# Kernel optimization log

Hardware: AMD Instinct MI355X
Metric: run time of the kernel (lower is better)

## Reference

```python
import jax, jax.numpy as jnp
import numpy as np

NUM_HEADS = 16
KEY_DIM = 64
EPS = 1e-6


def setup_inputs() -> dict:
    key = jax.random.key(0)
    k0, k1, k2, k3, k4 = jax.random.split(key, 5)
    B, S, E = 4, 4096, NUM_HEADS * KEY_DIM
    scale = 1.0 / np.sqrt(KEY_DIM)
    return {
        "query": jax.random.normal(k0, (B, S, E), dtype=jnp.float32),
        "Wq": jax.random.normal(k1, (NUM_HEADS, KEY_DIM, KEY_DIM), dtype=jnp.float32) * scale,
        "Wk": jax.random.normal(k2, (NUM_HEADS, KEY_DIM, KEY_DIM), dtype=jnp.float32) * scale,
        "Wv": jax.random.normal(k3, (NUM_HEADS, KEY_DIM, KEY_DIM), dtype=jnp.float32) * scale,
        "Wo": jax.random.normal(k4, (E, E), dtype=jnp.float32) * (1.0 / np.sqrt(E)),
    }


def reference(query, Wq, Wk, Wv, Wo):
    # Self-attention: key = value = query (per call() defaults).
    B, S, E = query.shape
    H, D = NUM_HEADS, KEY_DIM
    # split_heads: (B, S, E) -> (B, H, S, D)
    x = jnp.transpose(query.reshape(B, S, H, D), (0, 2, 1, 3))
    # Per-head linear projections (all heads batched in one einsum each).
    q = jnp.einsum("bhsd,hde->bhse", x, Wq)
    k = jnp.einsum("bhsd,hde->bhse", x, Wk)
    v = jnp.einsum("bhsd,hde->bhse", x, Wv)
    # Kernel feature map phi(x) = elu(x) + 1 (strictly positive).
    phi_q = jax.nn.elu(q) + 1.0
    phi_k = jax.nn.elu(k) + 1.0
    # Linear (non-causal) attention: O(S*D^2) instead of O(S^2*D).
    kv = jnp.einsum("bhsd,bhse->bhde", phi_k, v)        # (B,H,D,D)
    k_sum = jnp.sum(phi_k, axis=2)                       # (B,H,D)
    z = jnp.einsum("bhsd,bhd->bhs", phi_q, k_sum)        # (B,H,S)
    ctx = jnp.einsum("bhsd,bhde->bhse", phi_q, kv) / (z[..., None] + EPS)
    # combine_heads: (B,H,S,D) -> (B,S,E), then output projection (no bias).
    combined = jnp.transpose(ctx, (0, 2, 1, 3)).reshape(B, S, H * D)
    return combined @ Wo
```

## Files before the change

kernel.cpp:

```cpp
#include <hip/hip_runtime.h>
#include <stdint.h>

#define S_LEN 4096
#define NHEADS 16
#define DHEAD 64
#define EMB 1024
#define NBATCH 4
#define NBH (NBATCH * NHEADS)

typedef unsigned short u16t;
typedef __attribute__((ext_vector_type(8))) short short8;
typedef __attribute__((ext_vector_type(4))) float f32x4;

__device__ __forceinline__ u16t f2bf(float f) {
  unsigned int x = __float_as_uint(f);
  x += 0x7fffu + ((x >> 16) & 1u);
  return (u16t)(x >> 16);
}
__device__ __forceinline__ unsigned int pack2(float a, float b) {
  return (unsigned int)f2bf(a) | ((unsigned int)f2bf(b) << 16);
}
__device__ __forceinline__ float bf2f(u16t u) { return __uint_as_float(((unsigned int)u) << 16); }
__device__ __forceinline__ float phifn(float v) { return v > 0.f ? v + 1.f : __expf(v); }

__device__ __forceinline__ void stage_w8k(const u16t* __restrict__ wg,
                                          u16t* __restrict__ lds, int t) {
#pragma unroll
  for (int c = 0; c < 2; ++c) {
    const u16t* src = wg + (size_t)(c * 256 + t) * 8;
    char* dst = (char*)lds + c * 4096 + ((t >> 6) << 10);
    __builtin_amdgcn_global_load_lds((const __attribute__((address_space(1))) unsigned int*)src,
                                     (__attribute__((address_space(3))) unsigned int*)dst,
                                     16, 0, 0);
  }
}

__global__ __launch_bounds__(256) void la_wprep(const float* __restrict__ Wq,
                                                const float* __restrict__ Wk,
                                                const float* __restrict__ Wv,
                                                const float* __restrict__ Wo,
                                                u16t* __restrict__ WqT,
                                                u16t* __restrict__ WkT,
                                                u16t* __restrict__ WvT,
                                                u16t* __restrict__ WoT) {
  __shared__ float tmp[64][65];
  int blk = blockIdx.x;
  int t = threadIdx.x;
  if (blk < 48) {
    int mat = blk >> 4, h = blk & 15;
    const float* src = (mat == 0 ? Wq : (mat == 1 ? Wk : Wv)) + (size_t)h * 4096;
    u16t* dst = (mat == 0 ? WqT : (mat == 1 ? WkT : WvT)) + (size_t)h * 4096;
#pragma unroll
    for (int p = 0; p < 16; ++p) {
      int i = p * 256 + t;
      tmp[i >> 6][i & 63] = src[i];
    }
    __syncthreads();
#pragma unroll
    for (int p = 0; p < 16; ++p) {
      int i = p * 256 + t;
      int e = i >> 6, r = i & 63, o = r >> 3, j = r & 7;
      dst[i] = f2bf(tmp[((o ^ (e & 7)) << 3) + j][e]);
    }
  } else {
    int bb = blk - 48;
    int n0 = (bb & 15) * 64, k0 = (bb >> 4) * 64;
    int tx = t & 63, ty = t >> 6;
    for (int r = ty; r < 64; r += 4) tmp[r][tx] = Wo[(size_t)(k0 + r) * EMB + n0 + tx];
    __syncthreads();
    for (int r = ty; r < 64; r += 4)
      WoT[(size_t)(n0 + r) * EMB + k0 + tx] = f2bf(tmp[tx][r]);
  }
}

__global__ __launch_bounds__(256) void la_kvq5(const float* __restrict__ q,
                                               const u16t* __restrict__ WqT,
                                               const u16t* __restrict__ WkT,
                                               const u16t* __restrict__ WvT,
                                               u16t* __restrict__ phiq,
                                               float* __restrict__ kvpart,
                                               float* __restrict__ kspart) {
  __shared__ u16t xs[64 * 72];
  __shared__ u16t wq[4096];
  __shared__ u16t wk[4096];
  __shared__ u16t wv[4096];
  __shared__ u16t pkT[64 * 72];
  __shared__ u16t vT[64 * 72];
  __shared__ float ksp4[4][64];
  int blk = blockIdx.x;
  int bh = blk >> 3, tile = blk & 7;
  int b = bh >> 4, h = bh & 15;
  int s0 = tile << 9;
  int t = threadIdx.x;
  int wave = t >> 6, lane = t & 63, l16 = lane & 15, g = lane >> 4;

  stage_w8k(WqT + (size_t)h * 4096, wq, t);
  stage_w8k(WkT + (size_t)h * 4096, wk, t);
  stage_w8k(WvT + (size_t)h * 4096, wv, t);

  const float* xg = q + ((size_t)b * S_LEN + s0) * EMB + h * 64;
  int pr_r = t >> 4, pr_c4 = (t & 15) * 4;

  float4 pre[4];
#pragma unroll
  for (int i = 0; i < 4; ++i)
    pre[i] = *(const float4*)(xg + (size_t)(i * 16 + pr_r) * EMB + pr_c4);

  f32x4 kacc[4];
#pragma unroll
  for (int n = 0; n < 4; ++n) kacc[n] = 0.f;
  float ks_acc = 0.f;
  int ks_e = t & 63, ks_q = t >> 6;

  for (int c = 0; c < 8; ++c) {
    if (c) __syncthreads();
#pragma unroll
    for (int i = 0; i < 4; ++i) {
      uint2 p;
      p.x = pack2(pre[i].x, pre[i].y);
      p.y = pack2(pre[i].z, pre[i].w);
      *(uint2*)(&xs[(i * 16 + pr_r) * 72 + pr_c4]) = p;
    }
    if (c < 7) {
#pragma unroll
      for (int i = 0; i < 4; ++i)
        pre[i] = *(const float4*)(xg + (size_t)((c + 1) * 64 + i * 16 + pr_r) * EMB + pr_c4);
    }
    __syncthreads();

    f32x4 aQ[4], aK[4], aV[4];
#pragma unroll
    for (int n = 0; n < 4; ++n) { aQ[n] = 0.f; aK[n] = 0.f; aV[n] = 0.f; }
    short8 af[2];
#pragma unroll
    for (int kk = 0; kk < 2; ++kk)
      af[kk] = *(const short8*)(&xs[(wave * 16 + l16) * 72 + kk * 32 + g * 8]);
#pragma unroll
    for (int n = 0; n < 4; ++n) {
      int e = n * 16 + l16;
#pragma unroll
      for (int kk = 0; kk < 2; ++kk) {
        int op = (kk * 4 + g) ^ (l16 & 7);
        short8 bQ = *(const short8*)(&wq[e * 64 + op * 8]);
        short8 bK = *(const short8*)(&wk[e * 64 + op * 8]);
        short8 bV = *(const short8*)(&wv[e * 64 + op * 8]);
        aQ[n] = __builtin_amdgcn_mfma_f32_16x16x32_bf16(af[kk], bQ, aQ[n], 0, 0, 0);
        aK[n] = __builtin_amdgcn_mfma_f32_16x16x32_bf16(af[kk], bK, aK[n], 0, 0, 0);
        aV[n] = __builtin_amdgcn_mfma_f32_16x16x32_bf16(af[kk], bV, aV[n], 0, 0, 0);
      }
    }
    __syncthreads();

#pragma unroll
    for (int n = 0; n < 4; ++n) {
      int e = n * 16 + l16;
      int sb = wave * 16 + g * 4;
      uint2 pk2, vv2;
      pk2.x = pack2(phifn(aK[n][0]), phifn(aK[n][1]));
      pk2.y = pack2(phifn(aK[n][2]), phifn(aK[n][3]));
      vv2.x = pack2(aV[n][0], aV[n][1]);
      vv2.y = pack2(aV[n][2], aV[n][3]);
      *(uint2*)(&pkT[e * 72 + sb]) = pk2;
      *(uint2*)(&vT[e * 72 + sb]) = vv2;
#pragma unroll
      for (int j = 0; j < 4; ++j) xs[(sb + j) * 72 + e] = f2bf(phifn(aQ[n][j]));
    }
    __syncthreads();

#pragma unroll
    for (int i = 0; i < 2; ++i) {
      int slot = i * 256 + t;
      int r = slot >> 3, cc = (slot & 7) * 8;
      *(uint4*)(phiq + ((size_t)bh * S_LEN + s0 + c * 64 + r) * 64 + cc) =
          *(const uint4*)(&xs[r * 72 + cc]);
    }
#pragma unroll
    for (int ks = 0; ks < 2; ++ks) {
      short8 pa = *(const short8*)(&pkT[(wave * 16 + l16) * 72 + ks * 32 + g * 8]);
#pragma unroll
      for (int n = 0; n < 4; ++n) {
        short8 vb = *(const short8*)(&vT[(n * 16 + l16) * 72 + ks * 32 + g * 8]);
        kacc[n] = __builtin_amdgcn_mfma_f32_16x16x32_bf16(pa, vb, kacc[n], 0, 0, 0);
      }
    }
#pragma unroll
    for (int i = 0; i < 4; ++i) {
      uint2 u = *(const uint2*)(&pkT[ks_e * 72 + ks_q * 16 + i * 4]);
      ks_acc += bf2f((u16t)(u.x & 0xffff)) + bf2f((u16t)(u.x >> 16)) +
                bf2f((u16t)(u.y & 0xffff)) + bf2f((u16t)(u.y >> 16));
    }
  }

  float* kp = kvpart + (size_t)blk * 4096;
#pragma unroll
  for (int n = 0; n < 4; ++n)
#pragma unroll
    for (int j = 0; j < 4; ++j)
      kp[(wave * 16 + g * 4 + j) * 64 + n * 16 + l16] = kacc[n][j];

  ksp4[ks_q][ks_e] = ks_acc;
  __syncthreads();
  if (t < 64)
    kspart[(size_t)blk * 64 + t] = ksp4[0][t] + ksp4[1][t] + ksp4[2][t] + ksp4[3][t];
}

__global__ __launch_bounds__(256) void la_red3(const float* __restrict__ kvpart,
                                               const float* __restrict__ kspart,
                                               const u16t* __restrict__ WoT,
                                               float* __restrict__ ksum_g,
                                               u16t* __restrict__ W2T) {
  __shared__ float kvs[64][65];
  __shared__ u16t aT[256 * 72];
  int bh = blockIdx.x;
  int b = bh >> 4, h = bh & 15;
  int t = threadIdx.x, wave = t >> 6, lane = t & 63, l16 = lane & 15, g = lane >> 4;

  float acc[16];
#pragma unroll
  for (int i = 0; i < 16; ++i) acc[i] = 0.f;
  for (int p = 0; p < 8; ++p) {
    const float* base = kvpart + ((size_t)bh * 8 + p) * 4096;
#pragma unroll
    for (int i = 0; i < 16; ++i) acc[i] += base[i * 256 + t];
  }
#pragma unroll
  for (int i = 0; i < 16; ++i) {
    int idx = i * 256 + t;
    kvs[idx >> 6][idx & 63] = acc[i];
  }
  if (t < 64) {
    float a = 0.f;
    for (int p = 0; p < 8; ++p) a += kspart[((size_t)bh * 8 + p) * 64 + t];
    ksum_g[(size_t)bh * 64 + t] = a;
  }
  __syncthreads();

  short8 kvbf[4][2];
#pragma unroll
  for (int n = 0; n < 4; ++n)
#pragma unroll
    for (int kk = 0; kk < 2; ++kk) {
      u16t* pp = (u16t*)&kvbf[n][kk];
#pragma unroll
      for (int i = 0; i < 8; ++i) pp[i] = f2bf(kvs[n * 16 + l16][kk * 32 + g * 8 + i]);
    }

  for (int ec = 0; ec < 4; ++ec) {
    if (ec) __syncthreads();
#pragma unroll
    for (int p = 0; p < 8; ++p) {
      int slot = p * 256 + t;
      int r = slot >> 3, cc = (slot & 7) * 8;
      *(uint4*)(&aT[r * 72 + cc]) =
          *(const uint4*)(WoT + (size_t)(ec * 256 + r) * 1024 + h * 64 + cc);
    }
    __syncthreads();
    f32x4 c2[4][4];
#pragma unroll
    for (int mi = 0; mi < 4; ++mi)
#pragma unroll
      for (int n = 0; n < 4; ++n) c2[mi][n] = 0.f;
#pragma unroll
    for (int kk = 0; kk < 2; ++kk)
#pragma unroll
      for (int mi = 0; mi < 4; ++mi) {
        short8 afr = *(const short8*)(&aT[(wave * 64 + mi * 16 + l16) * 72 + kk * 32 + g * 8]);
#pragma unroll
        for (int n = 0; n < 4; ++n)
          c2[mi][n] = __builtin_amdgcn_mfma_f32_16x16x32_bf16(afr, kvbf[n][kk], c2[mi][n], 0, 0, 0);
      }
    __syncthreads();
#pragma unroll
    for (int mi = 0; mi < 4; ++mi)
#pragma unroll
      for (int n = 0; n < 4; ++n)
#pragma unroll
        for (int j = 0; j < 4; ++j)
          aT[(wave * 64 + mi * 16 + g * 4 + j) * 72 + n * 16 + l16] = f2bf(c2[mi][n][j]);
    __syncthreads();
#pragma unroll
    for (int p = 0; p < 8; ++p) {
      int slot = p * 256 + t;
      int r = slot >> 3, cc = (slot & 7) * 8;
      *(uint4*)(W2T + ((size_t)b << 20) + (size_t)(ec * 256 + r) * 1024 + h * 64 + cc) =
          *(const uint4*)(&aT[r * 72 + cc]);
    }
  }
}

__global__ __launch_bounds__(256) void la_scale(const u16t* __restrict__ phiq,
                                                const float* __restrict__ ksum_g,
                                                u16t* __restrict__ phiq2) {
  __shared__ float ks[64];
  int blk = blockIdx.x;
  int bh = blk >> 4, sl = blk & 15;
  int b = bh >> 4, h = bh & 15;
  int s0 = sl * 256;
  int t = threadIdx.x;
  if (t < 64) ks[t] = ksum_g[(size_t)bh * 64 + t];
  __syncthreads();
  int c16 = t & 15, rg = t >> 4;
#pragma unroll 2
  for (int it = 0; it < 16; ++it) {
    int s = s0 + it * 16 + rg;
    uint2 u = *(const uint2*)(phiq + ((size_t)bh * S_LEN + s) * 64 + c16 * 4);
    float f0 = bf2f((u16t)(u.x & 0xffff)), f1 = bf2f((u16t)(u.x >> 16));
    float f2 = bf2f((u16t)(u.y & 0xffff)), f3 = bf2f((u16t)(u.y >> 16));
    float zp = f0 * ks[c16 * 4] + f1 * ks[c16 * 4 + 1] + f2 * ks[c16 * 4 + 2] + f3 * ks[c16 * 4 + 3];
    zp += __shfl_xor(zp, 1);
    zp += __shfl_xor(zp, 2);
    zp += __shfl_xor(zp, 4);
    zp += __shfl_xor(zp, 8);
    float inv = 1.f / (zp + 1e-6f);
    uint2 o;
    o.x = pack2(f0 * inv, f1 * inv);
    o.y = pack2(f2 * inv, f3 * inv);
    *(uint2*)(phiq2 + ((size_t)(b * S_LEN + s)) * EMB + h * 64 + c16 * 4) = o;
  }
}

__device__ __forceinline__ void stage_half(const u16t* __restrict__ gbase,
                                           u16t* __restrict__ lbuf,
                                           int half, int t) {
#pragma unroll
  for (int it = 0; it < 2; ++it) {
    int slot = it * 512 + t;
    int row = half * 128 + (slot >> 3);
    int oct = slot & 7;
    const u16t* src = gbase + (size_t)row * EMB + (((oct ^ (row & 7)) << 3));
    char* dst = (char*)lbuf + ((half * 128 + it * 64 + ((t >> 6) << 3)) << 7);
    __builtin_amdgcn_global_load_lds((const __attribute__((address_space(1))) unsigned int*)src,
                                     (__attribute__((address_space(3))) unsigned int*)dst,
                                     16, 0, 0);
  }
}

#define GFENCE asm volatile("" ::: "memory")

#define LOAD_A(QM)                                                              \
  _Pragma("unroll") for (int mi = 0; mi < 4; ++mi) _Pragma("unroll")            \
      for (int kk = 0; kk < 2; ++kk) {                                          \
    int rr = (QM) * 128 + wr2 * 64 + mi * 16 + l16;                             \
    afr[mi][kk] = *(const short8*)((const char*)Acur + rr * 128 +               \
                                   ((((kk << 2) | g) ^ (rr & 7)) << 4));        \
  }
#define LOAD_B(QN, DST)                                                         \
  _Pragma("unroll") for (int ni = 0; ni < 2; ++ni) _Pragma("unroll")            \
      for (int kk = 0; kk < 2; ++kk) {                                          \
    int rr = (QN) * 128 + wc2 * 32 + ni * 16 + l16;                             \
    DST[ni][kk] = *(const short8*)((const char*)Bcur + rr * 128 +               \
                                   ((((kk << 2) | g) ^ (rr & 7)) << 4));        \
  }
#define MFMA_Q(QM, QN, BF)                                                      \
  __builtin_amdgcn_s_setprio(1);                                                \
  _Pragma("unroll") for (int mi = 0; mi < 4; ++mi) _Pragma("unroll")            \
      for (int ni = 0; ni < 2; ++ni) {                                          \
    acc[QM][QN][mi][ni] = __builtin_amdgcn_mfma_f32_16x16x32_bf16(              \
        afr[mi][0], BF[ni][0], acc[QM][QN][mi][ni], 0, 0, 0);                   \
    acc[QM][QN][mi][ni] = __builtin_amdgcn_mfma_f32_16x16x32_bf16(              \
        afr[mi][1], BF[ni][1], acc[QM][QN][mi][ni], 0, 0, 0);                   \
  }                                                                             \
  __builtin_amdgcn_s_setprio(0);

#define BAR()                      \
  __builtin_amdgcn_s_barrier();    \
  GFENCE

__global__ __launch_bounds__(512, 2) void la_gemm9(const u16t* __restrict__ A,
                                                   const u16t* __restrict__ W2T,
                                                   float* __restrict__ C) {
  __shared__ u16t SMEM[65536];
  u16t* Al0 = SMEM;
  u16t* Al1 = SMEM + 16384;
  u16t* Bl0 = SMEM + 32768;
  u16t* Bl1 = SMEM + 49152;
  int t = threadIdx.x;
  int bid = blockIdx.x;
  int swz = ((bid & 7) << 5) + (bid >> 3);
  int mt = swz >> 2, nt = swz & 3;
  const int M0 = mt * 256, N0 = nt * 256;
  const int b = mt >> 4;
  int wave = t >> 6, lane = t & 63;
  int l16 = lane & 15, g = lane >> 4;
  int wr2 = wave >> 2, wc2 = wave & 3;

  f32x4 acc[2][2][4][2];
#pragma unroll
  for (int qm = 0; qm < 2; ++qm)
#pragma unroll
    for (int qn = 0; qn < 2; ++qn)
#pragma unroll
      for (int mi = 0; mi < 4; ++mi)
#pragma unroll
        for (int ni = 0; ni < 2; ++ni) acc[qm][qn][mi][ni] = 0.f;

  const u16t* Asrc = A + (size_t)M0 * EMB;
  const u16t* Bsrc = W2T + ((size_t)b << 20) + (size_t)N0 * EMB;

  stage_half(Asrc, Al0, 0, t);
  stage_half(Bsrc, Bl0, 0, t);
  stage_half(Bsrc, Bl0, 1, t);
  stage_half(Asrc, Al0, 1, t);
  asm volatile("s_waitcnt vmcnt(4)" ::: "memory");
  BAR();

  short8 afr[4][2], bf0[2][2], bf1[2][2];

  for (int kt = 0; kt < 15; ++kt) {
    const u16t* Acur = (kt & 1) ? Al1 : Al0;
    const u16t* Bcur = (kt & 1) ? Bl1 : Bl0;
    u16t* Anxt = (kt & 1) ? Al0 : Al1;
    u16t* Bnxt = (kt & 1) ? Bl0 : Bl1;
    const u16t* An = Asrc + (kt + 1) * 64;
    const u16t* Bn = Bsrc + (kt + 1) * 64;
    LOAD_A(0);
    LOAD_B(0, bf0);
    stage_half(An, Anxt, 0, t);
    stage_half(Bn, Bnxt, 0, t);
    asm volatile("s_waitcnt vmcnt(6)" ::: "memory");
    BAR();
    MFMA_Q(0, 0, bf0);
    GFENCE;
    BAR();
    LOAD_B(1, bf1);
    stage_half(Bn, Bnxt, 1, t);
    asm volatile("s_waitcnt vmcnt(6)" ::: "memory");
    BAR();
    MFMA_Q(0, 1, bf1);
    GFENCE;
    BAR();
    LOAD_A(1);
    stage_half(An, Anxt, 1, t);
    BAR();
    MFMA_Q(1, 1, bf1);
    GFENCE;
    BAR();
    asm volatile("s_waitcnt vmcnt(4)" ::: "memory");
    BAR();
    MFMA_Q(1, 0, bf0);
    GFENCE;
    BAR();
  }
  {
    const u16t* Acur = Al1;
    const u16t* Bcur = Bl1;
    LOAD_A(0);
    LOAD_B(0, bf0);
    asm volatile("s_waitcnt vmcnt(2)" ::: "memory");
    BAR();
    MFMA_Q(0, 0, bf0);
    GFENCE;
    BAR();
    LOAD_B(1, bf1);
    asm volatile("s_waitcnt vmcnt(0)" ::: "memory");
    BAR();
    MFMA_Q(0, 1, bf1);
    GFENCE;
    BAR();
    LOAD_A(1);
    BAR();
    MFMA_Q(1, 1, bf1);
    GFENCE;
    BAR();
    BAR();
    MFMA_Q(1, 0, bf0);
    GFENCE;
  }

  float* cs = (float*)SMEM;
  BAR();
#pragma unroll
  for (int qq = 0; qq < 4; ++qq) {
    int qm = qq >> 1, qn = qq & 1;
#pragma unroll
    for (int mi = 0; mi < 4; ++mi)
#pragma unroll
      for (int ni = 0; ni < 2; ++ni)
#pragma unroll
        for (int j = 0; j < 4; ++j) {
          int row = wr2 * 64 + mi * 16 + g * 4 + j;
          int col = wc2 * 32 + ni * 16 + l16;
          cs[row * 132 + col] = acc[qm][qn][mi][ni][j];
        }
    BAR();
#pragma unroll
    for (int i = 0; i < 8; ++i) {
      int slot = i * 512 + t;
      int r = slot >> 5, sg = slot & 31;
      float4 v = *(const float4*)(&cs[r * 132 + sg * 4]);
      *(float4*)(&C[(size_t)(M0 + qm * 128 + r) * EMB + N0 + qn * 128 + sg * 4]) = v;
    }
    BAR();
  }
}

extern "C" void kernel_launch(void* const* d_in, const int* in_sizes, int n_in,
                              void* d_out, int out_size, void* d_ws, size_t ws_size,
                              hipStream_t stream) {
  const float* query = (const float*)d_in[0];
  const float* Wq = (const float*)d_in[1];
  const float* Wk = (const float*)d_in[2];
  const float* Wv = (const float*)d_in[3];
  const float* Wo = (const float*)d_in[4];
  float* out = (float*)d_out;
  char* ws = (char*)d_ws;

  u16t* WoT     = (u16t*)(ws);
  u16t* WqT     = (u16t*)(ws + 2097152);
  u16t* WkT     = (u16t*)(ws + 2228224);
  u16t* WvT     = (u16t*)(ws + 2359296);
  u16t* phiq    = (u16t*)(ws + 2490368);
  float* kvpart = (float*)(ws + 36044800);
  float* kspart = (float*)(ws + 44433408);
  float* ksum_g = (float*)(ws + 44564480);
  u16t* W2T     = (u16t*)(ws + 44580864);
  u16t* phiq2   = (u16t*)(ws + 52969472);

  la_wprep<<<304, 256, 0, stream>>>(Wq, Wk, Wv, Wo, WqT, WkT, WvT, WoT);
  la_kvq5<<<512, 256, 0, stream>>>(query, WqT, WkT, WvT, phiq, kvpart, kspart);
  la_red3<<<NBH, 256, 0, stream>>>(kvpart, kspart, WoT, ksum_g, W2T);
  la_scale<<<1024, 256, 0, stream>>>(phiq, ksum_g, phiq2);
  la_gemm9<<<256, 512, 0, stream>>>(phiq2, W2T, out);
}
```

Measured before the change: 106.7 us.

## Simplify GEMM main loop to one-stage prefetch with full-tile fragment loads

Replaces the quadrant-interleaved ping-pong schedule of the final GEMM with a simpler loop. Each iteration issues the global-to-LDS prefetch for the whole next K tile, waits for the current tile, loads all A and B fragments into registers, then runs all 32 MFMAs. This cuts the barriers per iteration from about eight to two and removes the peeled tail. The cost is higher register pressure from holding twice the fragments, and MFMA work no longer overlaps with LDS reads inside an iteration.

```diff
diff --git a/kernel.cpp b/kernel.cpp
--- a/kernel.cpp
+++ b/kernel.cpp
@@ -336,39 +336,13 @@
 }
 
 #define GFENCE asm volatile("" ::: "memory")
-
-#define LOAD_A(QM)                                                              \
-  _Pragma("unroll") for (int mi = 0; mi < 4; ++mi) _Pragma("unroll")            \
-      for (int kk = 0; kk < 2; ++kk) {                                          \
-    int rr = (QM) * 128 + wr2 * 64 + mi * 16 + l16;                             \
-    afr[mi][kk] = *(const short8*)((const char*)Acur + rr * 128 +               \
-                                   ((((kk << 2) | g) ^ (rr & 7)) << 4));        \
-  }
-#define LOAD_B(QN, DST)                                                         \
-  _Pragma("unroll") for (int ni = 0; ni < 2; ++ni) _Pragma("unroll")            \
-      for (int kk = 0; kk < 2; ++kk) {                                          \
-    int rr = (QN) * 128 + wc2 * 32 + ni * 16 + l16;                             \
-    DST[ni][kk] = *(const short8*)((const char*)Bcur + rr * 128 +               \
-                                   ((((kk << 2) | g) ^ (rr & 7)) << 4));        \
-  }
-#define MFMA_Q(QM, QN, BF)                                                      \
-  __builtin_amdgcn_s_setprio(1);                                                \
-  _Pragma("unroll") for (int mi = 0; mi < 4; ++mi) _Pragma("unroll")            \
-      for (int ni = 0; ni < 2; ++ni) {                                          \
-    acc[QM][QN][mi][ni] = __builtin_amdgcn_mfma_f32_16x16x32_bf16(              \
-        afr[mi][0], BF[ni][0], acc[QM][QN][mi][ni], 0, 0, 0);                   \
-    acc[QM][QN][mi][ni] = __builtin_amdgcn_mfma_f32_16x16x32_bf16(              \
-        afr[mi][1], BF[ni][1], acc[QM][QN][mi][ni], 0, 0, 0);                   \
-  }                                                                             \
-  __builtin_amdgcn_s_setprio(0);
-
 #define BAR()                      \
   __builtin_amdgcn_s_barrier();    \
   GFENCE
 
-__global__ __launch_bounds__(512, 2) void la_gemm9(const u16t* __restrict__ A,
-                                                   const u16t* __restrict__ W2T,
-                                                   float* __restrict__ C) {
+__global__ __launch_bounds__(512, 2) void la_gemm12(const u16t* __restrict__ A,
+                                                    const u16t* __restrict__ W2T,
+                                                    float* __restrict__ C) {
   __shared__ u16t SMEM[65536];
   u16t* Al0 = SMEM;
   u16t* Al1 = SMEM + 16384;
@@ -398,77 +372,76 @@
   const u16t* Bsrc = W2T + ((size_t)b << 20) + (size_t)N0 * EMB;
 
   stage_half(Asrc, Al0, 0, t);
+  stage_half(Asrc, Al0, 1, t);
   stage_half(Bsrc, Bl0, 0, t);
   stage_half(Bsrc, Bl0, 1, t);
-  stage_half(Asrc, Al0, 1, t);
-  asm volatile("s_waitcnt vmcnt(4)" ::: "memory");
-  BAR();
-
-  short8 afr[4][2], bf0[2][2], bf1[2][2];
-
-  for (int kt = 0; kt < 15; ++kt) {
+
+  short8 afr0[4][2], afr1[4][2], bfr0[2][2], bfr1[2][2];
+
+  for (int kt = 0; kt < 16; ++kt) {
     const u16t* Acur = (kt & 1) ? Al1 : Al0;
     const u16t* Bcur = (kt & 1) ? Bl1 : Bl0;
     u16t* Anxt = (kt & 1) ? Al0 : Al1;
     u16t* Bnxt = (kt & 1) ? Bl0 : Bl1;
-    const u16t* An = Asrc + (kt + 1) * 64;
-    const u16t* Bn = Bsrc + (kt + 1) * 64;
-    LOAD_A(0);
-    LOAD_B(0, bf0);
-    stage_half(An, Anxt, 0, t);
-    stage_half(Bn, Bnxt, 0, t);
-    asm volatile("s_waitcnt vmcnt(6)" ::: "memory");
+    if (kt < 15) {
+      const u16t* An = Asrc + (kt + 1) * 64;
+      const u16t* Bn = Bsrc + (kt + 1) * 64;
+      stage_half(An, Anxt, 0, t);
+      stage_half(An, Anxt, 1, t);
+      stage_half(Bn, Bnxt, 0, t);
+      stage_half(Bn, Bnxt, 1, t);
+      asm volatile("s_waitcnt vmcnt(8)" ::: "memory");
+    } else {
+      asm volatile("s_waitcnt vmcnt(0)" ::: "memory");
+    }
     BAR();
-    MFMA_Q(0, 0, bf0);
+
+#pragma unroll
+    for (int mi = 0; mi < 4; ++mi)
+#pragma unroll
+      for (int kk = 0; kk < 2; ++kk) {
+        int r0 = wr2 * 64 + mi * 16 + l16;
+        afr0[mi][kk] = *(const short8*)((const char*)Acur + r0 * 128 +
+                                        ((((kk << 2) | g) ^ (r0 & 7)) << 4));
+        int r1 = 128 + wr2 * 64 + mi * 16 + l16;
+        afr1[mi][kk] = *(const short8*)((const char*)Acur + r1 * 128 +
+                                        ((((kk << 2) | g) ^ (r1 & 7)) << 4));
+      }
+#pragma unroll
+    for (int ni = 0; ni < 2; ++ni)
+#pragma unroll
+      for (int kk = 0; kk < 2; ++kk) {
+        int r0 = wc2 * 32 + ni * 16 + l16;
+        bfr0[ni][kk] = *(const short8*)((const char*)Bcur + r0 * 128 +
+                                        ((((kk << 2) | g) ^ (r0 & 7)) << 4));
+        int r1 = 128 + wc2 * 32 + ni * 16 + l16;
+        bfr1[ni][kk] = *(const short8*)((const char*)Bcur + r1 * 128 +
+                                        ((((kk << 2) | g) ^ (r1 & 7)) << 4));
+      }
+
+    __builtin_amdgcn_s_setprio(1);
+#pragma unroll
+    for (int mi = 0; mi < 4; ++mi)
+#pragma unroll
+      for (int ni = 0; ni < 2; ++ni) {
+#pragma unroll
+        for (int kk = 0; kk < 2; ++kk) {
+          acc[0][0][mi][ni] = __builtin_amdgcn_mfma_f32_16x16x32_bf16(
+              afr0[mi][kk], bfr0[ni][kk], acc[0][0][mi][ni], 0, 0, 0);
+          acc[0][1][mi][ni] = __builtin_amdgcn_mfma_f32_16x16x32_bf16(
+              afr0[mi][kk], bfr1[ni][kk], acc[0][1][mi][ni], 0, 0, 0);
+          acc[1][0][mi][ni] = __builtin_amdgcn_mfma_f32_16x16x32_bf16(
+              afr1[mi][kk], bfr0[ni][kk], acc[1][0][mi][ni], 0, 0, 0);
+          acc[1][1][mi][ni] = __builtin_amdgcn_mfma_f32_16x16x32_bf16(
+              afr1[mi][kk], bfr1[ni][kk], acc[1][1][mi][ni], 0, 0, 0);
+        }
+      }
+    __builtin_amdgcn_s_setprio(0);
     GFENCE;
     BAR();
-    LOAD_B(1, bf1);
-    stage_half(Bn, Bnxt, 1, t);
-    asm volatile("s_waitcnt vmcnt(6)" ::: "memory");
-    BAR();
-    MFMA_Q(0, 1, bf1);
-    GFENCE;
-    BAR();
-    LOAD_A(1);
-    stage_half(An, Anxt, 1, t);
-    BAR();
-    MFMA_Q(1, 1, bf1);
-    GFENCE;
-    BAR();
-    asm volatile("s_waitcnt vmcnt(4)" ::: "memory");
-    BAR();
-    MFMA_Q(1, 0, bf0);
-    GFENCE;
-    BAR();
-  }
-  {
-    const u16t* Acur = Al1;
-    const u16t* Bcur = Bl1;
-    LOAD_A(0);
-    LOAD_B(0, bf0);
-    asm volatile("s_waitcnt vmcnt(2)" ::: "memory");
-    BAR();
-    MFMA_Q(0, 0, bf0);
-    GFENCE;
-    BAR();
-    LOAD_B(1, bf1);
-    asm volatile("s_waitcnt vmcnt(0)" ::: "memory");
-    BAR();
-    MFMA_Q(0, 1, bf1);
-    GFENCE;
-    BAR();
-    LOAD_A(1);
-    BAR();
-    MFMA_Q(1, 1, bf1);
-    GFENCE;
-    BAR();
-    BAR();
-    MFMA_Q(1, 0, bf0);
-    GFENCE;
   }
 
   float* cs = (float*)SMEM;
-  BAR();
 #pragma unroll
   for (int qq = 0; qq < 4; ++qq) {
     int qm = qq >> 1, qn = qq & 1;
@@ -520,5 +493,5 @@
   la_kvq5<<<512, 256, 0, stream>>>(query, WqT, WkT, WvT, phiq, kvpart, kspart);
   la_red3<<<NBH, 256, 0, stream>>>(kvpart, kspart, WoT, ksum_g, W2T);
   la_scale<<<1024, 256, 0, stream>>>(phiq, ksum_g, phiq2);
-  la_gemm9<<<256, 512, 0, stream>>>(phiq2, W2T, out);
-}
+  la_gemm12<<<256, 512, 0, stream>>>(phiq2, W2T, out);
+}
```

Result: no change. 107.9 us (+1.1%).

## Merge kv reduction and q scaling kernels, store GEMM output directly

Applied to the files above, without the earlier changes.

Fuses the kv/Wo folding kernel and the phi_q normalization kernel into one launch with 1088 blocks. The first 1024 blocks scale phi_q and reduce k_sum locally, and the last 64 blocks build W2T, removing one launch and the ksum_g round trip. The final GEMM now writes accumulators straight to global memory instead of staging through LDS for coalesced float4 stores. This drops barriers and LDS traffic but gives scattered 4-byte stores. The fused kernel's shared memory footprint is the larger branch for all blocks, which may reduce occupancy of the scaling blocks.

```diff
diff --git a/kernel.cpp b/kernel.cpp
--- a/kernel.cpp
+++ b/kernel.cpp
@@ -204,118 +204,116 @@
     kspart[(size_t)blk * 64 + t] = ksp4[0][t] + ksp4[1][t] + ksp4[2][t] + ksp4[3][t];
 }
 
-__global__ __launch_bounds__(256) void la_red3(const float* __restrict__ kvpart,
-                                               const float* __restrict__ kspart,
-                                               const u16t* __restrict__ WoT,
-                                               float* __restrict__ ksum_g,
-                                               u16t* __restrict__ W2T) {
-  __shared__ float kvs[64][65];
-  __shared__ u16t aT[256 * 72];
-  int bh = blockIdx.x;
-  int b = bh >> 4, h = bh & 15;
-  int t = threadIdx.x, wave = t >> 6, lane = t & 63, l16 = lane & 15, g = lane >> 4;
-
-  float acc[16];
-#pragma unroll
-  for (int i = 0; i < 16; ++i) acc[i] = 0.f;
-  for (int p = 0; p < 8; ++p) {
-    const float* base = kvpart + ((size_t)bh * 8 + p) * 4096;
-#pragma unroll
-    for (int i = 0; i < 16; ++i) acc[i] += base[i * 256 + t];
-  }
-#pragma unroll
-  for (int i = 0; i < 16; ++i) {
-    int idx = i * 256 + t;
-    kvs[idx >> 6][idx & 63] = acc[i];
-  }
-  if (t < 64) {
-    float a = 0.f;
-    for (int p = 0; p < 8; ++p) a += kspart[((size_t)bh * 8 + p) * 64 + t];
-    ksum_g[(size_t)bh * 64 + t] = a;
-  }
-  __syncthreads();
-
-  short8 kvbf[4][2];
-#pragma unroll
-  for (int n = 0; n < 4; ++n)
-#pragma unroll
-    for (int kk = 0; kk < 2; ++kk) {
-      u16t* pp = (u16t*)&kvbf[n][kk];
-#pragma unroll
-      for (int i = 0; i < 8; ++i) pp[i] = f2bf(kvs[n * 16 + l16][kk * 32 + g * 8 + i]);
-    }
-
-  for (int ec = 0; ec < 4; ++ec) {
-    if (ec) __syncthreads();
-#pragma unroll
+__global__ __launch_bounds__(256) void la_rs(const float* __restrict__ kvpart,
+                                             const float* __restrict__ kspart,
+                                             const u16t* __restrict__ WoT,
+                                             const u16t* __restrict__ phiq,
+                                             u16t* __restrict__ W2T,
+                                             u16t* __restrict__ phiq2) {
+  int blk = blockIdx.x;
+  int t = threadIdx.x;
+  if (blk < 1024) {
+    __shared__ float ks[64];
+    int bh = blk >> 4, sl = blk & 15;
+    int b = bh >> 4, h = bh & 15;
+    int s0 = sl * 256;
+    if (t < 64) {
+      float a = 0.f;
+      for (int p = 0; p < 8; ++p) a += kspart[((size_t)bh * 8 + p) * 64 + t];
+      ks[t] = a;
+    }
+    __syncthreads();
+    int c16 = t & 15, rg = t >> 4;
+#pragma unroll 2
+    for (int it = 0; it < 16; ++it) {
+      int s = s0 + it * 16 + rg;
+      uint2 u = *(const uint2*)(phiq + ((size_t)bh * S_LEN + s) * 64 + c16 * 4);
+      float f0 = bf2f((u16t)(u.x & 0xffff)), f1 = bf2f((u16t)(u.x >> 16));
+      float f2 = bf2f((u16t)(u.y & 0xffff)), f3 = bf2f((u16t)(u.y >> 16));
+      float zp = f0 * ks[c16 * 4] + f1 * ks[c16 * 4 + 1] + f2 * ks[c16 * 4 + 2] + f3 * ks[c16 * 4 + 3];
+      zp += __shfl_xor(zp, 1);
+      zp += __shfl_xor(zp, 2);
+      zp += __shfl_xor(zp, 4);
+      zp += __shfl_xor(zp, 8);
+      float inv = 1.f / (zp + 1e-6f);
+      uint2 o;
+      o.x = pack2(f0 * inv, f1 * inv);
+      o.y = pack2(f2 * inv, f3 * inv);
+      *(uint2*)(phiq2 + ((size_t)(b * S_LEN + s)) * EMB + h * 64 + c16 * 4) = o;
+    }
+  } else {
+    __shared__ float kvs[64][65];
+    __shared__ u16t aT[256 * 72];
+    int bh = blk - 1024;
+    int b = bh >> 4, h = bh & 15;
+    int wave = t >> 6, lane = t & 63, l16 = lane & 15, g = lane >> 4;
+
+    float acc[16];
+#pragma unroll
+    for (int i = 0; i < 16; ++i) acc[i] = 0.f;
     for (int p = 0; p < 8; ++p) {
-      int slot = p * 256 + t;
-      int r = slot >> 3, cc = (slot & 7) * 8;
-      *(uint4*)(&aT[r * 72 + cc]) =
-          *(const uint4*)(WoT + (size_t)(ec * 256 + r) * 1024 + h * 64 + cc);
-    }
-    __syncthreads();
-    f32x4 c2[4][4];
-#pragma unroll
-    for (int mi = 0; mi < 4; ++mi)
-#pragma unroll
-      for (int n = 0; n < 4; ++n) c2[mi][n] = 0.f;
-#pragma unroll
-    for (int kk = 0; kk < 2; ++kk)
-#pragma unroll
-      for (int mi = 0; mi < 4; ++mi) {
-        short8 afr = *(const short8*)(&aT[(wave * 64 + mi * 16 + l16) * 72 + kk * 32 + g * 8]);
+      const float* base = kvpart + ((size_t)bh * 8 + p) * 4096;
+#pragma unroll
+      for (int i = 0; i < 16; ++i) acc[i] += base[i * 256 + t];
+    }
+#pragma unroll
+    for (int i = 0; i < 16; ++i) {
+      int idx = i * 256 + t;
+      kvs[idx >> 6][idx & 63] = acc[i];
+    }
+    __syncthreads();
+
+    short8 kvbf[4][2];
+#pragma unroll
+    for (int n = 0; n < 4; ++n)
+#pragma unroll
+      for (int kk = 0; kk < 2; ++kk) {
+        u16t* pp = (u16t*)&kvbf[n][kk];
+#pragma unroll
+        for (int i = 0; i < 8; ++i) pp[i] = f2bf(kvs[n * 16 + l16][kk * 32 + g * 8 + i]);
+      }
+
+    for (int ec = 0; ec < 4; ++ec) {
+      if (ec) __syncthreads();
+#pragma unroll
+      for (int p = 0; p < 8; ++p) {
+        int slot = p * 256 + t;
+        int r = slot >> 3, cc = (slot & 7) * 8;
+        *(uint4*)(&aT[r * 72 + cc]) =
+            *(const uint4*)(WoT + (size_t)(ec * 256 + r) * 1024 + h * 64 + cc);
+      }
+      __syncthreads();
+      f32x4 c2[4][4];
+#pragma unroll
+      for (int mi = 0; mi < 4; ++mi)
+#pragma unroll
+        for (int n = 0; n < 4; ++n) c2[mi][n] = 0.f;
+#pragma unroll
+      for (int kk = 0; kk < 2; ++kk)
+#pragma unroll
+        for (int mi = 0; mi < 4; ++mi) {
+          short8 afr = *(const short8*)(&aT[(wave * 64 + mi * 16 + l16) * 72 + kk * 32 + g * 8]);
+#pragma unroll
+          for (int n = 0; n < 4; ++n)
+            c2[mi][n] = __builtin_amdgcn_mfma_f32_16x16x32_bf16(afr, kvbf[n][kk], c2[mi][n], 0, 0, 0);
+        }
+      __syncthreads();
+#pragma unroll
+      for (int mi = 0; mi < 4; ++mi)
 #pragma unroll
         for (int n = 0; n < 4; ++n)
-          c2[mi][n] = __builtin_amdgcn_mfma_f32_16x16x32_bf16(afr, kvbf[n][kk], c2[mi][n], 0, 0, 0);
+#pragma unroll
+          for (int j = 0; j < 4; ++j)
+            aT[(wave * 64 + mi * 16 + g * 4 + j) * 72 + n * 16 + l16] = f2bf(c2[mi][n][j]);
+      __syncthreads();
+#pragma unroll
+      for (int p = 0; p < 8; ++p) {
+        int slot = p * 256 + t;
+        int r = slot >> 3, cc = (slot & 7) * 8;
+        *(uint4*)(W2T + ((size_t)b << 20) + (size_t)(ec * 256 + r) * 1024 + h * 64 + cc) =
+            *(const uint4*)(&aT[r * 72 + cc]);
       }
-    __syncthreads();
-#pragma unroll
-    for (int mi = 0; mi < 4; ++mi)
-#pragma unroll
-      for (int n = 0; n < 4; ++n)
-#pragma unroll
-        for (int j = 0; j < 4; ++j)
-          aT[(wave * 64 + mi * 16 + g * 4 + j) * 72 + n * 16 + l16] = f2bf(c2[mi][n][j]);
-    __syncthreads();
-#pragma unroll
-    for (int p = 0; p < 8; ++p) {
-      int slot = p * 256 + t;
-      int r = slot >> 3, cc = (slot & 7) * 8;
-      *(uint4*)(W2T + ((size_t)b << 20) + (size_t)(ec * 256 + r) * 1024 + h * 64 + cc) =
-          *(const uint4*)(&aT[r * 72 + cc]);
-    }
-  }
-}
-
-__global__ __launch_bounds__(256) void la_scale(const u16t* __restrict__ phiq,
-                                                const float* __restrict__ ksum_g,
-                                                u16t* __restrict__ phiq2) {
-  __shared__ float ks[64];
-  int blk = blockIdx.x;
-  int bh = blk >> 4, sl = blk & 15;
-  int b = bh >> 4, h = bh & 15;
-  int s0 = sl * 256;
-  int t = threadIdx.x;
-  if (t < 64) ks[t] = ksum_g[(size_t)bh * 64 + t];
-  __syncthreads();
-  int c16 = t & 15, rg = t >> 4;
-#pragma unroll 2
-  for (int it = 0; it < 16; ++it) {
-    int s = s0 + it * 16 + rg;
-    uint2 u = *(const uint2*)(phiq + ((size_t)bh * S_LEN + s) * 64 + c16 * 4);
-    float f0 = bf2f((u16t)(u.x & 0xffff)), f1 = bf2f((u16t)(u.x >> 16));
-    float f2 = bf2f((u16t)(u.y & 0xffff)), f3 = bf2f((u16t)(u.y >> 16));
-    float zp = f0 * ks[c16 * 4] + f1 * ks[c16 * 4 + 1] + f2 * ks[c16 * 4 + 2] + f3 * ks[c16 * 4 + 3];
-    zp += __shfl_xor(zp, 1);
-    zp += __shfl_xor(zp, 2);
-    zp += __shfl_xor(zp, 4);
-    zp += __shfl_xor(zp, 8);
-    float inv = 1.f / (zp + 1e-6f);
-    uint2 o;
-    o.x = pack2(f0 * inv, f1 * inv);
-    o.y = pack2(f2 * inv, f3 * inv);
-    *(uint2*)(phiq2 + ((size_t)(b * S_LEN + s)) * EMB + h * 64 + c16 * 4) = o;
+    }
   }
 }
 
@@ -369,11 +367,8 @@
 __global__ __launch_bounds__(512, 2) void la_gemm9(const u16t* __restrict__ A,
                                                    const u16t* __restrict__ W2T,
                                                    float* __restrict__ C) {
-  __shared__ u16t SMEM[65536];
-  u16t* Al0 = SMEM;
-  u16t* Al1 = SMEM + 16384;
-  u16t* Bl0 = SMEM + 32768;
-  u16t* Bl1 = SMEM + 49152;
+  __shared__ u16t Al[2][16384];
+  __shared__ u16t Bl[2][16384];
   int t = threadIdx.x;
   int bid = blockIdx.x;
   int swz = ((bid & 7) << 5) + (bid >> 3);
@@ -397,20 +392,20 @@
   const u16t* Asrc = A + (size_t)M0 * EMB;
   const u16t* Bsrc = W2T + ((size_t)b << 20) + (size_t)N0 * EMB;
 
-  stage_half(Asrc, Al0, 0, t);
-  stage_half(Bsrc, Bl0, 0, t);
-  stage_half(Bsrc, Bl0, 1, t);
-  stage_half(Asrc, Al0, 1, t);
+  stage_half(Asrc, Al[0], 0, t);
+  stage_half(Bsrc, Bl[0], 0, t);
+  stage_half(Bsrc, Bl[0], 1, t);
+  stage_half(Asrc, Al[0], 1, t);
   asm volatile("s_waitcnt vmcnt(4)" ::: "memory");
   BAR();
 
   short8 afr[4][2], bf0[2][2], bf1[2][2];
 
   for (int kt = 0; kt < 15; ++kt) {
-    const u16t* Acur = (kt & 1) ? Al1 : Al0;
-    const u16t* Bcur = (kt & 1) ? Bl1 : Bl0;
-    u16t* Anxt = (kt & 1) ? Al0 : Al1;
-    u16t* Bnxt = (kt & 1) ? Bl0 : Bl1;
+    const u16t* Acur = Al[kt & 1];
+    const u16t* Bcur = Bl[kt & 1];
+    u16t* Anxt = Al[(kt + 1) & 1];
+    u16t* Bnxt = Bl[(kt + 1) & 1];
     const u16t* An = Asrc + (kt + 1) * 64;
     const u16t* Bn = Bsrc + (kt + 1) * 64;
     LOAD_A(0);
@@ -442,8 +437,8 @@
     BAR();
   }
   {
-    const u16t* Acur = Al1;
-    const u16t* Bcur = Bl1;
+    const u16t* Acur = Al[1];
+    const u16t* Bcur = Bl[1];
     LOAD_A(0);
     LOAD_B(0, bf0);
     asm volatile("s_waitcnt vmcnt(2)" ::: "memory");
@@ -467,31 +462,20 @@
     GFENCE;
   }
 
-  float* cs = (float*)SMEM;
-  BAR();
-#pragma unroll
-  for (int qq = 0; qq < 4; ++qq) {
-    int qm = qq >> 1, qn = qq & 1;
-#pragma unroll
-    for (int mi = 0; mi < 4; ++mi)
-#pragma unroll
-      for (int ni = 0; ni < 2; ++ni)
-#pragma unroll
-        for (int j = 0; j < 4; ++j) {
-          int row = wr2 * 64 + mi * 16 + g * 4 + j;
-          int col = wc2 * 32 + ni * 16 + l16;
-          cs[row * 132 + col] = acc[qm][qn][mi][ni][j];
-        }
-    BAR();
-#pragma unroll
-    for (int i = 0; i < 8; ++i) {
-      int slot = i * 512 + t;
-      int r = slot >> 5, sg = slot & 31;
-      float4 v = *(const float4*)(&cs[r * 132 + sg * 4]);
-      *(float4*)(&C[(size_t)(M0 + qm * 128 + r) * EMB + N0 + qn * 128 + sg * 4]) = v;
-    }
-    BAR();
-  }
+#pragma unroll
+  for (int qm = 0; qm < 2; ++qm)
+#pragma unroll
+    for (int qn = 0; qn < 2; ++qn)
+#pragma unroll
+      for (int mi = 0; mi < 4; ++mi)
+#pragma unroll
+        for (int ni = 0; ni < 2; ++ni)
+#pragma unroll
+          for (int j = 0; j < 4; ++j) {
+            int row = M0 + qm * 128 + wr2 * 64 + mi * 16 + g * 4 + j;
+            int col = N0 + qn * 128 + wc2 * 32 + ni * 16 + l16;
+            C[(size_t)row * EMB + col] = acc[qm][qn][mi][ni][j];
+          }
 }
 
 extern "C" void kernel_launch(void* const* d_in, const int* in_sizes, int n_in,
@@ -512,13 +496,11 @@
   u16t* phiq    = (u16t*)(ws + 2490368);
   float* kvpart = (float*)(ws + 36044800);
   float* kspart = (float*)(ws + 44433408);
-  float* ksum_g = (float*)(ws + 44564480);
-  u16t* W2T     = (u16t*)(ws + 44580864);
-  u16t* phiq2   = (u16t*)(ws + 52969472);
+  u16t* W2T     = (u16t*)(ws + 44564480);
+  u16t* phiq2   = (u16t*)(ws + 52953088);
 
   la_wprep<<<304, 256, 0, stream>>>(Wq, Wk, Wv, Wo, WqT, WkT, WvT, WoT);
   la_kvq5<<<512, 256, 0, stream>>>(query, WqT, WkT, WvT, phiq, kvpart, kspart);
-  la_red3<<<NBH, 256, 0, stream>>>(kvpart, kspart, WoT, ksum_g, W2T);
-  la_scale<<<1024, 256, 0, stream>>>(phiq, ksum_g, phiq2);
+  la_rs<<<1088, 256, 0, stream>>>(kvpart, kspart, WoT, phiq, W2T, phiq2);
   la_gemm9<<<256, 512, 0, stream>>>(phiq2, W2T, out);
 }
```

Measured after the change: 122.3 us. 1.15x slower.
